# Kernel tuning notes

Hardware: AMD Instinct MI355X
Metric: run time of the kernel (lower is better)

The kernel has to match this reference:

```python
import jax, jax.numpy as jnp
import numpy as np

# 5-tap image-gradient filter (cross-correlation taps, as in F.conv2d)
_K5 = (-1.0 / 12.0, 2.0 / 3.0, 0.0, -2.0 / 3.0, 1.0 / 12.0)
ALPHA = BETA = GAMMA = DELTA = 1.0
MASK_COST = 1.0
ENTROPY_WEIGHT = 1.0


def _pen(x):
    return jnp.sqrt(x + 1e-5)


def _filt_w(x):
    # depthwise 1x5 filter along W, padding 2 (matches F.conv2d(x, kernel_gx, padding=(0,2)))
    W = x.shape[-1]
    xp = jnp.pad(x, ((0, 0), (0, 0), (0, 0), (2, 2)))
    out = _K5[0] * xp[..., 0:W]
    for j in range(1, 5):
        out = out + _K5[j] * xp[..., j:j + W]
    return out


def _filt_h(x):
    # depthwise 5x1 filter along H, padding 2
    H = x.shape[-2]
    xp = jnp.pad(x, ((0, 0), (0, 0), (2, 2), (0, 0)))
    out = _K5[0] * xp[..., 0:H, :]
    for j in range(1, 5):
        out = out + _K5[j] * xp[..., j:j + H, :]
    return out


def _warp(img, flow):
    # Bilinear warp: sample img at (x + flow_x, y + flow_y); out-of-range taps contribute 0
    B, C, H, W = img.shape
    xq = jnp.arange(W, dtype=img.dtype)[None, None, :] + flow[:, 0]  # (B,H,W)
    yq = jnp.arange(H, dtype=img.dtype)[None, :, None] + flow[:, 1]
    x0 = jnp.floor(xq)
    y0 = jnp.floor(yq)
    wx1 = xq - x0
    wy1 = yq - y0
    img_flat = img.reshape(B, C, H * W)

    def tap(xi, yi, w):
        valid = (xi >= 0) & (xi <= W - 1) & (yi >= 0) & (yi <= H - 1)
        xc = jnp.clip(xi, 0, W - 1).astype(jnp.int32)
        yc = jnp.clip(yi, 0, H - 1).astype(jnp.int32)
        idx = (yc * W + xc).reshape(B, 1, H * W)
        vals = jnp.take_along_axis(img_flat, jnp.broadcast_to(idx, (B, C, H * W)), axis=2)
        vals = vals.reshape(B, C, H, W)
        return vals * (w * valid.astype(img.dtype))[:, None]

    return (tap(x0, y0, (1 - wx1) * (1 - wy1)) + tap(x0 + 1, y0, wx1 * (1 - wy1))
            + tap(x0, y0 + 1, (1 - wx1) * wy1) + tap(x0 + 1, y0 + 1, wx1 * wy1))


def _border_mask(flow):
    B, _, H, W = flow.shape
    Xp = jnp.arange(W, dtype=flow.dtype)[None, None, :] + flow[:, 0]
    Yp = jnp.arange(H, dtype=flow.dtype)[None, :, None] + flow[:, 1]
    mask_x = jax.nn.sigmoid(Xp + 0.5) * (1.0 - jax.nn.sigmoid(Xp - (W - 0.5)))
    mask_y = jax.nn.sigmoid(Yp + 0.5) * (1.0 - jax.nn.sigmoid(Yp - (H - 0.5)))
    return mask_x * mask_y


def _direction_terms(flow_a, flow_b, img_a, img_b):
    # energy terms for one direction (warping *_b by flow_a)
    mask = _border_mask(flow_a)
    flow_b_warp = _warp(flow_b, flow_a)
    mag = jnp.sum(flow_a ** 2 + flow_b_warp ** 2, axis=1)
    diff = flow_a + flow_b_warp
    occ = 1.0 - jax.nn.sigmoid(jnp.sum(diff ** 2, axis=1) - (0.01 * mag + 0.5))
    mask = mask * occ
    mask_term = MASK_COST * jnp.sum(1.0 - mask, axis=(1, 2)).mean()
    img_b_warp = _warp(img_b, flow_a)
    A = jnp.sum((img_a - img_b_warp) ** 2, axis=1)
    data_term = ALPHA * jnp.sum(_pen(A) * mask, axis=(1, 2)).mean()
    dx = flow_a[..., 1:] - flow_a[..., :-1]
    dy = flow_a[:, :, 1:, :] - flow_a[:, :, :-1, :]
    Bt = (jnp.pad(jnp.sum(dx ** 2, axis=1), ((0, 0), (0, 0), (0, 1)))
          + jnp.pad(jnp.sum(dy ** 2, axis=1), ((0, 0), (0, 1), (0, 0))))
    smooth_term = BETA * jnp.sum(_pen(Bt), axis=(1, 2)).mean()
    Ct = (jnp.sum((_filt_w(img_a) - _filt_w(img_b_warp)) ** 2, axis=1)
          + jnp.sum((_filt_h(img_a) - _filt_h(img_b_warp)) ** 2, axis=1))
    grad_term = GAMMA * jnp.sum(_pen(Ct) * mask, axis=(1, 2)).mean()
    D = jnp.sum(diff ** 2, axis=1)
    fb_part = DELTA * jnp.sum(_pen(D) * mask, axis=(1, 2)).mean()
    return mask_term + data_term + smooth_term + grad_term + fb_part


def _elbo_epe(meanf, log_varf, meanb, log_varb, img1, img2, target, noise_f, noise_b):
    # reparameterized flow samples (Nsamples = 1)
    flowf = meanf + jnp.exp(log_varf / 2.0) * noise_f
    flowb = meanb + jnp.exp(log_varb / 2.0) * noise_b
    energy = (_direction_terms(flowf, flowb, img1, img2)
              + _direction_terms(flowb, flowf, img2, img1))
    entropy = (jnp.sum(log_varf, axis=(1, 2, 3)) / 2
               + jnp.sum(log_varb, axis=(1, 2, 3)) / 2).mean()
    elbo = energy - ENTROPY_WEIGHT * entropy
    epe = jnp.sqrt(jnp.sum((meanf - target) ** 2, axis=1)).mean()
    return elbo, epe


def setup_inputs() -> dict:
    key = jax.random.key(0)
    ks = jax.random.split(key, 9)
    B, H, W = 8, 384, 512
    return {
        "meanf": jax.random.normal(ks[0], (B, 2, H, W), jnp.float32),
        "log_varf": jax.random.normal(ks[1], (B, 2, H, W), jnp.float32),
        "meanb": jax.random.normal(ks[2], (B, 2, H, W), jnp.float32),
        "log_varb": jax.random.normal(ks[3], (B, 2, H, W), jnp.float32),
        "img1": jax.random.uniform(ks[4], (B, 3, H, W), jnp.float32),
        "img2": jax.random.uniform(ks[5], (B, 3, H, W), jnp.float32),
        "target": jax.random.normal(ks[6], (B, 2, H, W), jnp.float32),
        "noise_f": jax.random.normal(ks[7], (B, 2, H, W), jnp.float32),
        "noise_b": jax.random.normal(ks[8], (B, 2, H, W), jnp.float32),
    }


def reference(meanf, log_varf, meanb, log_varb, img1, img2, target, noise_f, noise_b):
    elbo, epe = _elbo_epe(meanf, log_varf, meanb, log_varb, img1, img2, target, noise_f, noise_b)
    return (elbo, epe)
```

## Files before the change

### kernel.cpp

```cpp
#include <hip/hip_runtime.h>
#include <math.h>

#define BATCH 8
#define IH 384
#define IW 512
#define NPIX (IH*IW)
#define BN (BATCH*NPIX)

#define TW 64
#define TH 16
#define RW (TW+4)
#define RH (TH+4)
#define NTX (IW/TW)
#define NTY (IH/TH)
#define NZ  (BATCH*2)
#define NB_DIR (NTX*NTY*NZ)

#define HSX 8
#define HSY 6
#define SH (TH+2*HSY)
#define SW (TW+2*HSX)
#define SF4 (SW/4)

#define NITER_A 4

#define NB_FLOW 1536
#define PA_OFF 0
#define PB_OFF NB_DIR
#define ENT_OFF (2*NB_DIR)
#define EPE_OFF (ENT_OFF + NB_FLOW)
#define PART_FLOATS 16384

__device__ __forceinline__ float frcp_(float x){ return __builtin_amdgcn_rcpf(x); }
__device__ __forceinline__ float fsqrt_(float x){ return __builtin_amdgcn_sqrtf(x); }
__device__ __forceinline__ float sigmoidf_(float x){ return frcp_(1.0f + __expf(-x)); }

__device__ __forceinline__ float block_reduce_sum(float v){
    __shared__ float s[8];
    #pragma unroll
    for (int off=32; off>0; off>>=1) v += __shfl_down(v, off);
    int lane = threadIdx.x & 63, wid = threadIdx.x >> 6;
    if (lane==0) s[wid] = v;
    __syncthreads();
    float t = 0.f;
    if (wid==0){
        int nw = (blockDim.x+63)>>6;
        t = (lane < nw) ? s[lane] : 0.f;
        #pragma unroll
        for (int off=4; off>0; off>>=1) t += __shfl_down(t, off);
    }
    __syncthreads();
    return t;
}

__global__ __launch_bounds__(256)
void flows_kernel(const float* __restrict__ meanf, const float* __restrict__ log_varf,
                  const float* __restrict__ meanb, const float* __restrict__ log_varb,
                  const float* __restrict__ target,
                  const float* __restrict__ noise_f, const float* __restrict__ noise_b,
                  float* __restrict__ flowf, float* __restrict__ flowb,
                  float* __restrict__ part)
{
    int t = blockIdx.x*blockDim.x + threadIdx.x;
    if (t < NB_DIR) part[PB_OFF + t] = 0.f;
    const int NP4 = NPIX/4;
    int b = t / NP4, p4 = t - b*NP4;
    size_t i0 = ((size_t)b*2*NPIX)/4 + p4;
    size_t i1 = i0 + NPIX/4;

    const float4* mf = (const float4*)meanf;  const float4* lf = (const float4*)log_varf;
    const float4* mb = (const float4*)meanb;  const float4* lb = (const float4*)log_varb;
    const float4* nf = (const float4*)noise_f; const float4* nb = (const float4*)noise_b;
    const float4* tg = (const float4*)target;
    float4* ff = (float4*)flowf; float4* fbp = (float4*)flowb;

    float4 lf0 = lf[i0], lf1 = lf[i1], lb0 = lb[i0], lb1 = lb[i1];
    float4 mf0 = mf[i0], mf1 = mf[i1], mb0 = mb[i0], mb1 = mb[i1];
    float4 nf0 = nf[i0], nf1 = nf[i1], nb0 = nb[i0], nb1 = nb[i1];

    float4 o;
    o.x = mf0.x + __expf(0.5f*lf0.x)*nf0.x; o.y = mf0.y + __expf(0.5f*lf0.y)*nf0.y;
    o.z = mf0.z + __expf(0.5f*lf0.z)*nf0.z; o.w = mf0.w + __expf(0.5f*lf0.w)*nf0.w;
    ff[i0] = o;
    o.x = mf1.x + __expf(0.5f*lf1.x)*nf1.x; o.y = mf1.y + __expf(0.5f*lf1.y)*nf1.y;
    o.z = mf1.z + __expf(0.5f*lf1.z)*nf1.z; o.w = mf1.w + __expf(0.5f*lf1.w)*nf1.w;
    ff[i1] = o;
    o.x = mb0.x + __expf(0.5f*lb0.x)*nb0.x; o.y = mb0.y + __expf(0.5f*lb0.y)*nb0.y;
    o.z = mb0.z + __expf(0.5f*lb0.z)*nb0.z; o.w = mb0.w + __expf(0.5f*lb0.w)*nb0.w;
    fbp[i0] = o;
    o.x = mb1.x + __expf(0.5f*lb1.x)*nb1.x; o.y = mb1.y + __expf(0.5f*lb1.y)*nb1.y;
    o.z = mb1.z + __expf(0.5f*lb1.z)*nb1.z; o.w = mb1.w + __expf(0.5f*lb1.w)*nb1.w;
    fbp[i1] = o;

    float ent = (lf0.x+lf0.y+lf0.z+lf0.w) + (lf1.x+lf1.y+lf1.z+lf1.w)
              + (lb0.x+lb0.y+lb0.z+lb0.w) + (lb1.x+lb1.y+lb1.z+lb1.w);

    float4 t0 = tg[i0], t1 = tg[i1];
    float d0, d1, epe = 0.f;
    d0 = mf0.x - t0.x; d1 = mf1.x - t1.x; epe += fsqrt_(d0*d0 + d1*d1);
    d0 = mf0.y - t0.y; d1 = mf1.y - t1.y; epe += fsqrt_(d0*d0 + d1*d1);
    d0 = mf0.z - t0.z; d1 = mf1.z - t1.z; epe += fsqrt_(d0*d0 + d1*d1);
    d0 = mf0.w - t0.w; d1 = mf1.w - t1.w; epe += fsqrt_(d0*d0 + d1*d1);

    float s = block_reduce_sum(ent);
    if (threadIdx.x == 0) part[ENT_OFF + blockIdx.x] = s;
    float s2 = block_reduce_sum(epe);
    if (threadIdx.x == 0) part[EPE_OFF + blockIdx.x] = s2;
}

struct FB8 { float v0,v1,v2,v3,v4,v5,v6,v7; };

__device__ __forceinline__ void tap_idx_(int gw, int gh, float fax, float fay,
                                         int& idx0, int& idx1, int& idx2, int& idx3)
{
    float Xp = (float)gw + fax;
    float Yp = (float)gh + fay;
    float x0f = floorf(Xp), y0f = floorf(Yp);
    float xc0 = fminf(fmaxf(x0f,       0.f), (float)(IW-1));
    float xc1 = fminf(fmaxf(x0f + 1.f, 0.f), (float)(IW-1));
    float yc0 = fminf(fmaxf(y0f,       0.f), (float)(IH-1));
    float yc1 = fminf(fmaxf(y0f + 1.f, 0.f), (float)(IH-1));
    int ix0 = (int)xc0, ix1 = (int)xc1, iy0 = (int)yc0, iy1 = (int)yc1;
    idx0 = iy0*IW + ix0; idx1 = iy0*IW + ix1;
    idx2 = iy1*IW + ix0; idx3 = iy1*IW + ix1;
}

__device__ __forceinline__ FB8 fb_load_(const float* __restrict__ pfb,
                                        int idx0, int idx1, int idx2, int idx3)
{
    const float* pfb1 = pfb + NPIX;
    FB8 r;
    r.v0 = pfb[idx0];  r.v1 = pfb[idx1];  r.v2 = pfb[idx2];  r.v3 = pfb[idx3];
    r.v4 = pfb1[idx0]; r.v5 = pfb1[idx1]; r.v6 = pfb1[idx2]; r.v7 = pfb1[idx3];
    return r;
}

__global__ __launch_bounds__(256, 6)
void dirA_kernel(const float* __restrict__ flowf, const float* __restrict__ flowb,
                 const float* __restrict__ img1, const float* __restrict__ img2,
                 float* __restrict__ wimg, float* __restrict__ maskbuf,
                 float* __restrict__ part)
{
    __shared__ float sib[3][SH][SW];

    const int z = blockIdx.z;
    const int dir = z & 1, b = z >> 1;
    const float *pfa, *pfb, *pia, *pib;
    if (dir == 0){ pfa = flowf; pfb = flowb; pia = img1; pib = img2; }
    else         { pfa = flowb; pfb = flowf; pia = img2; pib = img1; }
    pfa += (size_t)b*2*NPIX; pfb += (size_t)b*2*NPIX;
    pia += (size_t)b*3*NPIX; pib += (size_t)b*3*NPIX;

    float* wout = wimg + (size_t)z*3*NPIX;
    float* mout = maskbuf + (size_t)z*NPIX;

    const int tw0 = blockIdx.x*TW, th0 = blockIdx.y*TH;
    const int tid = threadIdx.x;
    const int hh0 = tid >> 6, ww0 = tid & 63;
    float local = 0.f;

    for (int i = tid; i < 3*SH*SF4; i += 256){
        int c = i / (SH*SF4);
        int rem = i - c*(SH*SF4);
        int r = rem / SF4, c4 = rem - r*SF4;
        int gy = th0 - HSY + r;
        int gx = tw0 - HSX + 4*c4;
        float4 v = make_float4(0.f, 0.f, 0.f, 0.f);
        if (gy >= 0 && gy < IH && gx >= 0 && gx < IW){
            v = *(const float4*)(pib + (size_t)c*NPIX + gy*IW + gx);
        }
        *(float4*)&sib[c][r][4*c4] = v;
    }

    float rfax[NITER_A], rfay[NITER_A];
    #pragma unroll
    for (int it = 0; it < NITER_A; ++it){
        int p = (th0 + hh0 + it*4)*IW + (tw0 + ww0);
        rfax[it] = pfa[p];
        rfay[it] = pfa[NPIX + p];
    }
    __syncthreads();

    FB8 fb_cur, fb_nxt;
    {
        int j0, j1, j2, j3;
        tap_idx_(tw0 + ww0, th0 + hh0, rfax[0], rfay[0], j0, j1, j2, j3);
        fb_cur = fb_load_(pfb, j0, j1, j2, j3);
    }

    #pragma unroll
    for (int it = 0; it < NITER_A; ++it){
        int hh = hh0 + it*4, ww = ww0;
        int gh = th0 + hh, gw = tw0 + ww;
        int p = gh*IW + gw;
        float fax = rfax[it], fay = rfay[it];

        if (it + 1 < NITER_A){
            int j0, j1, j2, j3;
            tap_idx_(gw, th0 + hh0 + (it+1)*4, rfax[it+1], rfay[it+1], j0, j1, j2, j3);
            fb_nxt = fb_load_(pfb, j0, j1, j2, j3);
        }

        float Xp = (float)gw + fax;
        float Yp = (float)gh + fay;

        float x0f = floorf(Xp), y0f = floorf(Yp);
        float wx1 = Xp - x0f, wy1 = Yp - y0f;
        float wx0 = 1.f - wx1, wy0 = 1.f - wy1;

        float x1f = x0f + 1.f, y1f = y0f + 1.f;
        bool vx0 = (x0f >= 0.f) && (x0f <= (float)(IW-1));
        bool vx1 = (x1f >= 0.f) && (x1f <= (float)(IW-1));
        bool vy0 = (y0f >= 0.f) && (y0f <= (float)(IH-1));
        bool vy1 = (y1f >= 0.f) && (y1f <= (float)(IH-1));
        float xc0 = fminf(fmaxf(x0f, 0.f), (float)(IW-1));
        float xc1 = fminf(fmaxf(x1f, 0.f), (float)(IW-1));
        float yc0 = fminf(fmaxf(y0f, 0.f), (float)(IH-1));
        float yc1 = fminf(fmaxf(y1f, 0.f), (float)(IH-1));
        int ix0 = (int)xc0, ix1 = (int)xc1, iy0 = (int)yc0, iy1 = (int)yc1;
        int idx0 = iy0*IW + ix0, idx1 = iy0*IW + ix1;
        int idx2 = iy1*IW + ix0, idx3 = iy1*IW + ix1;
        float wt0 = (vx0 && vy0) ? wx0*wy0 : 0.f;
        float wt1 = (vx1 && vy0) ? wx1*wy0 : 0.f;
        float wt2 = (vx0 && vy1) ? wx0*wy1 : 0.f;
        float wt3 = (vx1 && vy1) ? wx1*wy1 : 0.f;

        float w0, w1, w2;
        int lx0 = ix0 - (tw0 - HSX), ly0 = iy0 - (th0 - HSY);
        int lx1 = ix1 - (tw0 - HSX), ly1 = iy1 - (th0 - HSY);
        bool inwin = (lx0 >= 0) && (lx1 < SW) && (ly0 >= 0) && (ly1 < SH);
        if (inwin){
            int o00 = ly0*SW + lx0, o01 = ly0*SW + lx1;
            int o10 = ly1*SW + lx0, o11 = ly1*SW + lx1;
            const float* s0 = &sib[0][0][0];
            const float* s1 = s0 + SH*SW;
            const float* s2 = s1 + SH*SW;
            w0 = wt0*s0[o00] + wt1*s0[o01] + wt2*s0[o10] + wt3*s0[o11];
            w1 = wt0*s1[o00] + wt1*s1[o01] + wt2*s1[o10] + wt3*s1[o11];
            w2 = wt0*s2[o00] + wt1*s2[o01] + wt2*s2[o10] + wt3*s2[o11];
        } else {
            const float* g1 = pib + NPIX;
            const float* g2 = pib + 2*NPIX;
            w0 = wt0*pib[idx0] + wt1*pib[idx1] + wt2*pib[idx2] + wt3*pib[idx3];
            w1 = wt0*g1[idx0]  + wt1*g1[idx1]  + wt2*g1[idx2]  + wt3*g1[idx3];
            w2 = wt0*g2[idx0]  + wt1*g2[idx1]  + wt2*g2[idx2]  + wt3*g2[idx3];
        }

        float mx = sigmoidf_(Xp + 0.5f) * (1.f - sigmoidf_(Xp - ((float)IW - 0.5f)));
        float my = sigmoidf_(Yp + 0.5f) * (1.f - sigmoidf_(Yp - ((float)IH - 0.5f)));
        float bm = mx * my;

        float fbwx = wt0*fb_cur.v0 + wt1*fb_cur.v1 + wt2*fb_cur.v2 + wt3*fb_cur.v3;
        float fbwy = wt0*fb_cur.v4 + wt1*fb_cur.v5 + wt2*fb_cur.v6 + wt3*fb_cur.v7;

        float mag = fax*fax + fay*fay + fbwx*fbwx + fbwy*fbwy;
        float dfx = fax + fbwx, dfy = fay + fbwy;
        float D = dfx*dfx + dfy*dfy;
        float occ = 1.f - sigmoidf_(D - (0.01f*mag + 0.5f));
        float mask = bm * occ;

        local += (1.f - mask);

        float d0 = pia[p]        - w0;
        float d1 = pia[NPIX+p]   - w1;
        float d2 = pia[2*NPIX+p] - w2;
        local += fsqrt_(d0*d0 + d1*d1 + d2*d2 + 1e-5f) * mask;

        local += fsqrt_(D + 1e-5f) * mask;

        float Bt = 0.f;
        if (gw < IW-1){
            float e0 = pfa[p+1] - fax;
            float e1 = pfa[NPIX + p+1] - fay;
            Bt += e0*e0 + e1*e1;
        }
        if (gh < IH-1){
            float e0 = pfa[p+IW] - fax;
            float e1 = pfa[NPIX + p+IW] - fay;
            Bt += e0*e0 + e1*e1;
        }
        local += fsqrt_(Bt + 1e-5f);

        wout[p]          = w0;
        wout[NPIX + p]   = w1;
        wout[2*NPIX + p] = w2;
        mout[p]          = mask;

        if (it + 1 < NITER_A) fb_cur = fb_nxt;
    }

    float s = block_reduce_sum(local);
    if (tid == 0) part[PA_OFF + blockIdx.x + NTX*(blockIdx.y + NTY*blockIdx.z)] = s;
}

__global__ __launch_bounds__(256, 5)
void dirB_kernel(const float* __restrict__ img1, const float* __restrict__ img2,
                 const float* __restrict__ wimg, const float* __restrict__ maskbuf,
                 float* __restrict__ part)
{
    __shared__ float wt[3][RH][RW];
    __shared__ float at[3][RH][RW];

    const int z = blockIdx.z;
    const int dir = z & 1, b = z >> 1;
    const float* pia = ((dir == 0) ? img1 : img2) + (size_t)b*3*NPIX;
    const float* wsrc = wimg + (size_t)z*3*NPIX;
    const float* msrc = maskbuf + (size_t)z*NPIX;

    const int tw0 = blockIdx.x*TW, th0 = blockIdx.y*TH;
    const int tid = threadIdx.x;
    float local = 0.f;

    for (int i = tid; i < 3*RH*RW; i += 256){
        int c = i / (RH*RW);
        int rem = i - c*(RH*RW);
        int r = rem / RW, cc = rem - r*RW;
        int gy = th0 + r - 2;
        int gx = tw0 + cc - 2;
        float va = 0.f, vw = 0.f;
        if (gy >= 0 && gy < IH && gx >= 0 && gx < IW){
            size_t q = (size_t)c*NPIX + gy*IW + gx;
            va = pia[q];
            vw = wsrc[q];
        }
        at[c][r][cc] = va;
        wt[c][r][cc] = vw;
    }
    __syncthreads();

    const float K0 = -1.f/12.f, K1 = 2.f/3.f, K3 = -2.f/3.f, K4 = 1.f/12.f;
    #pragma unroll
    for (int it = 0; it < NITER_A; ++it){
        int i = tid + it*256;
        int hh = i >> 6, ww = i & 63;
        int p = (th0 + hh)*IW + (tw0 + ww);
        int lh = hh + 2, lw = ww + 2;
        float Ct = 0.f;
        #pragma unroll
        for (int c = 0; c < 3; ++c){
            float gxa = K0*at[c][lh][lw-2] + K1*at[c][lh][lw-1]
                      + K3*at[c][lh][lw+1] + K4*at[c][lh][lw+2];
            float gxw = K0*wt[c][lh][lw-2] + K1*wt[c][lh][lw-1]
                      + K3*wt[c][lh][lw+1] + K4*wt[c][lh][lw+2];
            float d = gxa - gxw; Ct += d*d;
            float gya = K0*at[c][lh-2][lw] + K1*at[c][lh-1][lw]
                      + K3*at[c][lh+1][lw] + K4*at[c][lh+2][lw];
            float gyw = K0*wt[c][lh-2][lw] + K1*wt[c][lh-1][lw]
                      + K3*wt[c][lh+1][lw] + K4*wt[c][lh+2][lw];
            d = gya - gyw; Ct += d*d;
        }
        local += fsqrt_(Ct + 1e-5f) * msrc[p];
    }

    float s = block_reduce_sum(local);
    if (tid == 0) part[PB_OFF + blockIdx.x + NTX*(blockIdx.y + NTY*blockIdx.z)] = s;
}

__global__ __launch_bounds__(256)
void finalize_kernel(const float* __restrict__ part, float* __restrict__ out)
{
    float e = 0.f, ent = 0.f, epe = 0.f;
    for (int i = threadIdx.x; i < 2*NB_DIR; i += 256) e += part[i];
    for (int i = threadIdx.x; i < NB_FLOW; i += 256){
        ent += part[ENT_OFF + i];
        epe += part[EPE_OFF + i];
    }
    e   = block_reduce_sum(e);
    ent = block_reduce_sum(ent);
    epe = block_reduce_sum(epe);
    if (threadIdx.x == 0){
        out[0] = e / (float)BATCH - ent / (2.f * (float)BATCH);
        out[1] = epe / ((float)BATCH * (float)NPIX);
    }
}

extern "C" void kernel_launch(void* const* d_in, const int* in_sizes, int n_in,
                              void* d_out, int out_size, void* d_ws, size_t ws_size,
                              hipStream_t stream)
{
    const float* meanf    = (const float*)d_in[0];
    const float* log_varf = (const float*)d_in[1];
    const float* meanb    = (const float*)d_in[2];
    const float* log_varb = (const float*)d_in[3];
    const float* img1     = (const float*)d_in[4];
    const float* img2     = (const float*)d_in[5];
    const float* target   = (const float*)d_in[6];
    const float* noise_f  = (const float*)d_in[7];
    const float* noise_b  = (const float*)d_in[8];

    float* ws    = (float*)d_ws;
    float* part  = ws;
    float* flowf = ws + PART_FLOATS;
    float* flowb = flowf + 2*(size_t)BN;
    float* wimg  = flowb + 2*(size_t)BN;
    float* maskb = wimg + (size_t)NZ*3*NPIX;

    const int threads = 256;

    flows_kernel<<<NB_FLOW, threads, 0, stream>>>(meanf, log_varf, meanb, log_varb,
                                                  target, noise_f, noise_b,
                                                  flowf, flowb, part);

    dim3 grid(NTX, NTY, NZ);
    dirA_kernel<<<grid, threads, 0, stream>>>(flowf, flowb, img1, img2,
                                              wimg, maskb, part);
    dirB_kernel<<<grid, threads, 0, stream>>>(img1, img2, wimg, maskb, part);

    finalize_kernel<<<1, threads, 0, stream>>>(part, (float*)d_out);
}
```

Measured before the change: 256.4 us.

## Stage backward-flow tile in LDS alongside warped image for bilinear gathers

Extends the shared-memory halo window in dirA_kernel from three image channels to five, adding the two backward-flow channels, so the flow gathers are served from LDS instead of prefetched global loads. The vertical halo shrinks from 6 to 4 rows to offset the extra LDS footprint, and launch bounds drop to 4 blocks per SIMD. This removes eight scattered global loads per pixel when taps land inside the window. In exchange, samples outside the narrower window take the slower global path more often, and occupancy is lower.

```diff
diff --git a/kernel.cpp b/kernel.cpp
--- a/kernel.cpp
+++ b/kernel.cpp
@@ -17,10 +17,11 @@
 #define NB_DIR (NTX*NTY*NZ)
 
 #define HSX 8
-#define HSY 6
+#define HSY 4
 #define SH (TH+2*HSY)
 #define SW (TW+2*HSX)
 #define SF4 (SW/4)
+#define NCH 5
 
 #define NITER_A 4
 
@@ -108,40 +109,13 @@
     if (threadIdx.x == 0) part[EPE_OFF + blockIdx.x] = s2;
 }
 
-struct FB8 { float v0,v1,v2,v3,v4,v5,v6,v7; };
-
-__device__ __forceinline__ void tap_idx_(int gw, int gh, float fax, float fay,
-                                         int& idx0, int& idx1, int& idx2, int& idx3)
-{
-    float Xp = (float)gw + fax;
-    float Yp = (float)gh + fay;
-    float x0f = floorf(Xp), y0f = floorf(Yp);
-    float xc0 = fminf(fmaxf(x0f,       0.f), (float)(IW-1));
-    float xc1 = fminf(fmaxf(x0f + 1.f, 0.f), (float)(IW-1));
-    float yc0 = fminf(fmaxf(y0f,       0.f), (float)(IH-1));
-    float yc1 = fminf(fmaxf(y0f + 1.f, 0.f), (float)(IH-1));
-    int ix0 = (int)xc0, ix1 = (int)xc1, iy0 = (int)yc0, iy1 = (int)yc1;
-    idx0 = iy0*IW + ix0; idx1 = iy0*IW + ix1;
-    idx2 = iy1*IW + ix0; idx3 = iy1*IW + ix1;
-}
-
-__device__ __forceinline__ FB8 fb_load_(const float* __restrict__ pfb,
-                                        int idx0, int idx1, int idx2, int idx3)
-{
-    const float* pfb1 = pfb + NPIX;
-    FB8 r;
-    r.v0 = pfb[idx0];  r.v1 = pfb[idx1];  r.v2 = pfb[idx2];  r.v3 = pfb[idx3];
-    r.v4 = pfb1[idx0]; r.v5 = pfb1[idx1]; r.v6 = pfb1[idx2]; r.v7 = pfb1[idx3];
-    return r;
-}
-
-__global__ __launch_bounds__(256, 6)
+__global__ __launch_bounds__(256, 4)
 void dirA_kernel(const float* __restrict__ flowf, const float* __restrict__ flowb,
                  const float* __restrict__ img1, const float* __restrict__ img2,
                  float* __restrict__ wimg, float* __restrict__ maskbuf,
                  float* __restrict__ part)
 {
-    __shared__ float sib[3][SH][SW];
+    __shared__ float sib[NCH][SH][SW];
 
     const int z = blockIdx.z;
     const int dir = z & 1, b = z >> 1;
@@ -156,10 +130,9 @@
 
     const int tw0 = blockIdx.x*TW, th0 = blockIdx.y*TH;
     const int tid = threadIdx.x;
-    const int hh0 = tid >> 6, ww0 = tid & 63;
     float local = 0.f;
 
-    for (int i = tid; i < 3*SH*SF4; i += 256){
+    for (int i = tid; i < NCH*SH*SF4; i += 256){
         int c = i / (SH*SF4);
         int rem = i - c*(SH*SF4);
         int r = rem / SF4, c4 = rem - r*SF4;
@@ -167,7 +140,9 @@
         int gx = tw0 - HSX + 4*c4;
         float4 v = make_float4(0.f, 0.f, 0.f, 0.f);
         if (gy >= 0 && gy < IH && gx >= 0 && gx < IW){
-            v = *(const float4*)(pib + (size_t)c*NPIX + gy*IW + gx);
+            const float* src = (c < 3) ? (pib + (size_t)c*NPIX)
+                                       : (pfb + (size_t)(c-3)*NPIX);
+            v = *(const float4*)(src + gy*IW + gx);
         }
         *(float4*)&sib[c][r][4*c4] = v;
     }
@@ -175,32 +150,21 @@
     float rfax[NITER_A], rfay[NITER_A];
     #pragma unroll
     for (int it = 0; it < NITER_A; ++it){
-        int p = (th0 + hh0 + it*4)*IW + (tw0 + ww0);
+        int i = tid + it*256;
+        int hh = i >> 6, ww = i & 63;
+        int p = (th0 + hh)*IW + (tw0 + ww);
         rfax[it] = pfa[p];
         rfay[it] = pfa[NPIX + p];
     }
     __syncthreads();
 
-    FB8 fb_cur, fb_nxt;
-    {
-        int j0, j1, j2, j3;
-        tap_idx_(tw0 + ww0, th0 + hh0, rfax[0], rfay[0], j0, j1, j2, j3);
-        fb_cur = fb_load_(pfb, j0, j1, j2, j3);
-    }
-
     #pragma unroll
     for (int it = 0; it < NITER_A; ++it){
-        int hh = hh0 + it*4, ww = ww0;
+        int i = tid + it*256;
+        int hh = i >> 6, ww = i & 63;
         int gh = th0 + hh, gw = tw0 + ww;
         int p = gh*IW + gw;
         float fax = rfax[it], fay = rfay[it];
-
-        if (it + 1 < NITER_A){
-            int j0, j1, j2, j3;
-            tap_idx_(gw, th0 + hh0 + (it+1)*4, rfax[it+1], rfay[it+1], j0, j1, j2, j3);
-            fb_nxt = fb_load_(pfb, j0, j1, j2, j3);
-        }
-
         float Xp = (float)gw + fax;
         float Yp = (float)gh + fay;
 
@@ -225,7 +189,7 @@
         float wt2 = (vx0 && vy1) ? wx0*wy1 : 0.f;
         float wt3 = (vx1 && vy1) ? wx1*wy1 : 0.f;
 
-        float w0, w1, w2;
+        float w0, w1, w2, fbwx, fbwy;
         int lx0 = ix0 - (tw0 - HSX), ly0 = iy0 - (th0 - HSY);
         int lx1 = ix1 - (tw0 - HSX), ly1 = iy1 - (th0 - HSY);
         bool inwin = (lx0 >= 0) && (lx1 < SW) && (ly0 >= 0) && (ly1 < SH);
@@ -235,23 +199,27 @@
             const float* s0 = &sib[0][0][0];
             const float* s1 = s0 + SH*SW;
             const float* s2 = s1 + SH*SW;
-            w0 = wt0*s0[o00] + wt1*s0[o01] + wt2*s0[o10] + wt3*s0[o11];
-            w1 = wt0*s1[o00] + wt1*s1[o01] + wt2*s1[o10] + wt3*s1[o11];
-            w2 = wt0*s2[o00] + wt1*s2[o01] + wt2*s2[o10] + wt3*s2[o11];
+            const float* s3 = s2 + SH*SW;
+            const float* s4 = s3 + SH*SW;
+            w0   = wt0*s0[o00] + wt1*s0[o01] + wt2*s0[o10] + wt3*s0[o11];
+            w1   = wt0*s1[o00] + wt1*s1[o01] + wt2*s1[o10] + wt3*s1[o11];
+            w2   = wt0*s2[o00] + wt1*s2[o01] + wt2*s2[o10] + wt3*s2[o11];
+            fbwx = wt0*s3[o00] + wt1*s3[o01] + wt2*s3[o10] + wt3*s3[o11];
+            fbwy = wt0*s4[o00] + wt1*s4[o01] + wt2*s4[o10] + wt3*s4[o11];
         } else {
             const float* g1 = pib + NPIX;
             const float* g2 = pib + 2*NPIX;
-            w0 = wt0*pib[idx0] + wt1*pib[idx1] + wt2*pib[idx2] + wt3*pib[idx3];
-            w1 = wt0*g1[idx0]  + wt1*g1[idx1]  + wt2*g1[idx2]  + wt3*g1[idx3];
-            w2 = wt0*g2[idx0]  + wt1*g2[idx1]  + wt2*g2[idx2]  + wt3*g2[idx3];
+            const float* pfb1 = pfb + NPIX;
+            w0   = wt0*pib[idx0] + wt1*pib[idx1] + wt2*pib[idx2] + wt3*pib[idx3];
+            w1   = wt0*g1[idx0]  + wt1*g1[idx1]  + wt2*g1[idx2]  + wt3*g1[idx3];
+            w2   = wt0*g2[idx0]  + wt1*g2[idx1]  + wt2*g2[idx2]  + wt3*g2[idx3];
+            fbwx = wt0*pfb[idx0] + wt1*pfb[idx1] + wt2*pfb[idx2] + wt3*pfb[idx3];
+            fbwy = wt0*pfb1[idx0]+ wt1*pfb1[idx1]+ wt2*pfb1[idx2]+ wt3*pfb1[idx3];
         }
 
         float mx = sigmoidf_(Xp + 0.5f) * (1.f - sigmoidf_(Xp - ((float)IW - 0.5f)));
         float my = sigmoidf_(Yp + 0.5f) * (1.f - sigmoidf_(Yp - ((float)IH - 0.5f)));
         float bm = mx * my;
-
-        float fbwx = wt0*fb_cur.v0 + wt1*fb_cur.v1 + wt2*fb_cur.v2 + wt3*fb_cur.v3;
-        float fbwy = wt0*fb_cur.v4 + wt1*fb_cur.v5 + wt2*fb_cur.v6 + wt3*fb_cur.v7;
 
         float mag = fax*fax + fay*fay + fbwx*fbwx + fbwy*fbwy;
         float dfx = fax + fbwx, dfy = fay + fbwy;
@@ -285,8 +253,6 @@
         wout[NPIX + p]   = w1;
         wout[2*NPIX + p] = w2;
         mout[p]          = mask;
-
-        if (it + 1 < NITER_A) fb_cur = fb_nxt;
     }
 
     float s = block_reduce_sum(local);
```

Measured after the change: 241.2 us. 5.9% less time.
